# Kernel tuning notes

Measured on AMD Instinct MI355X. Metric: run time of the kernel, lower is better.

Reference implementation:

```python
import jax, jax.numpy as jnp
import numpy as np

B, N_DET, N_T, NY, NX = 4, 128, 2048, 256, 256


def setup_inputs() -> dict:
    key = jax.random.key(0)
    k1, k2, k3 = jax.random.split(key, 3)
    sino = jax.random.normal(k1, (B, 1, N_DET, N_T), dtype=jnp.float32)
    # LUT channel 0: floor temporal index (stored as float, cast to int in forward)
    k_floor = jax.random.randint(k2, (NY, NX, N_DET), 0, N_T).astype(jnp.float32)
    # LUT channel 1: linear interpolation weight alpha in [0,1)
    alpha = jax.random.uniform(k3, (NY, NX, N_DET), dtype=jnp.float32)
    lut = jnp.stack([k_floor, alpha], axis=-1)  # [NY, NX, N_DET, 2]
    return {"sino": sino, "lut": lut}


def reference(sino, lut):
    # sino: [B, 1, n_det, n_t]; lut: [ny, nx, n_det, 2]
    b, c, n_det, n_t = sino.shape
    k_floor = lut[..., 0].astype(jnp.int32)          # [ny, nx, n_det]
    alpha = lut[..., 1]                               # [ny, nx, n_det]
    valid = (k_floor >= 0) & (k_floor < n_t - 1)
    k0 = jnp.clip(k_floor, 0, n_t - 2)
    k1 = k0 + 1
    S = sino[:, 0]                                    # [B, n_det, n_t]
    det = jnp.arange(n_det)                           # broadcasts against [ny,nx,n_det]
    s0 = S[:, det, k0]                                # [B, ny, nx, n_det]
    s1 = S[:, det, k1]                                # [B, ny, nx, n_det]
    sk = (1.0 - alpha) * s0 + alpha * s1
    sk = jnp.where(valid, sk, jnp.zeros_like(sk))
    # Hann apodization window over detectors
    apod = (0.5 - 0.5 * jnp.cos(2.0 * jnp.pi * jnp.arange(n_det, dtype=jnp.float32)
                                / max(n_det - 1, 1))).astype(sino.dtype)
    out = jnp.einsum('bijd,d->bij', sk, apod)
    norm = jnp.maximum(apod.sum(), 1e-06)
    out = out / norm
    return out[:, None]                               # [B, 1, ny, nx]
```

## Files before the change

kernel.cpp:

```cpp
#include <hip/hip_runtime.h>
#include <hip/hip_fp16.h>


#define NB      4
#define NDET    128
#define NT      2048
#define NPIX    65536
#define DPHASE  4
#define DBLOCK  8
#define PTILE   2048
#define THREADS 512
#define PXPT    (PTILE / THREADS)

__global__ __launch_bounds__(THREADS, 4)
void bp_kernel(const float* __restrict__ sino,
               const float* __restrict__ lut,
               float* __restrict__ out) {
    __shared__ __half lds[DPHASE * NT * NB];

    const int tid  = threadIdx.x;
    const int pair = blockIdx.x & 15;
    const int tile = blockIdx.x >> 4;
    const int d0   = pair * DBLOCK;
    const int px0  = tile * PTILE;

    float apod[DBLOCK];
#pragma unroll
    for (int j = 0; j < DBLOCK; ++j) {
        float x = (float)(d0 + j) * (6.28318530717958647692f / 127.0f);
        apod[j] = 0.5f - 0.5f * __cosf(x);
    }

    float acc[PXPT][NB];
#pragma unroll
    for (int i = 0; i < PXPT; ++i)
#pragma unroll
        for (int b = 0; b < NB; ++b) acc[i][b] = 0.0f;

    const float4* sino4 = (const float4*)sino;

    for (int phase = 0; phase < 2; ++phase) {
        const int dg0 = d0 + phase * DPHASE;
        if (phase) __syncthreads();

        for (int f = tid; f < DPHASE * NB * (NT / 4); f += THREADS) {
            int t4 = f & 511;
            int r  = f >> 9;
            int dl = r >> 2;
            int b  = r & 3;
            float4 v = sino4[((size_t)b * NDET + (dg0 + dl)) * (NT / 4) + t4];
            int t = t4 * 4;
            __half* dst = &lds[(dl * NT + t) * NB + b];
            dst[0 * NB] = __float2half(v.x);
            dst[1 * NB] = __float2half(v.y);
            dst[2 * NB] = __float2half(v.z);
            dst[3 * NB] = __float2half(v.w);
        }
        __syncthreads();

#pragma unroll
        for (int i = 0; i < PXPT; ++i) {
            const int px = px0 + tid + i * THREADS;
            const float4* lp = (const float4*)(lut + ((size_t)px * NDET + dg0) * 2);
            float4 L0 = lp[0];
            float4 L1 = lp[1];

            auto do_det = [&](float kf, float af, int dl, int j) {
                int k = (int)kf;
                unsigned uk = (unsigned)k;
                bool valid = uk < 2047u;
                float w  = valid ? apod[j] : 0.0f;
                int  k0  = valid ? k : 0;
                const __half2* q = (const __half2*)&lds[(dl * NT + k0) * NB];
                __half2 s0a = q[0], s0b = q[1];
                __half2 s1a = q[2], s1b = q[3];
                __half2 a2  = __float2half2_rn(af);
                __half2 ska = __hfma2(a2, __hsub2(s1a, s0a), s0a);
                __half2 skb = __hfma2(a2, __hsub2(s1b, s0b), s0b);
                float2 fa = __half22float2(ska);
                float2 fb = __half22float2(skb);
                acc[i][0] = fmaf(w, fa.x, acc[i][0]);
                acc[i][1] = fmaf(w, fa.y, acc[i][1]);
                acc[i][2] = fmaf(w, fb.x, acc[i][2]);
                acc[i][3] = fmaf(w, fb.y, acc[i][3]);
            };
            int jb = phase * DPHASE;
            do_det(L0.x, L0.y, 0, jb + 0);
            do_det(L0.z, L0.w, 1, jb + 1);
            do_det(L1.x, L1.y, 2, jb + 2);
            do_det(L1.z, L1.w, 3, jb + 3);
        }
    }

    const float inv_norm = 1.0f / 63.5f;
#pragma unroll
    for (int i = 0; i < PXPT; ++i) {
        const int px = px0 + tid + i * THREADS;
#pragma unroll
        for (int b = 0; b < NB; ++b) {
            atomicAdd(&out[(size_t)b * NPIX + px], acc[i][b] * inv_norm);
        }
    }
}

extern "C" void kernel_launch(void* const* d_in, const int* in_sizes, int n_in,
                              void* d_out, int out_size, void* d_ws, size_t ws_size,
                              hipStream_t stream) {
    const float* sino = (const float*)d_in[0];
    const float* lut  = (const float*)d_in[1];
    float* out = (float*)d_out;

    hipMemsetAsync(d_out, 0, (size_t)out_size * sizeof(float), stream);

    bp_kernel<<<dim3(512), dim3(THREADS), 0, stream>>>(sino, lut, out);
}
```

Measured before the change: 144.6 us.

## Prefetch LUT across phases, shrink LDS stage, remap blocks to XCDs

Each detector-phase stage now holds 2 detectors instead of 4 (16KB LDS instead of 32KB), which allows more resident blocks per CU. The next phase's LUT float4 is loaded into registers before the current phase's sinogram staging and compute, so the global LUT latency overlaps with LDS fill. Blocks are shrunk to 256 threads and 1024-pixel tiles, the grid is doubled to 1024, and block IDs are remapped so that each XCD handles two detector octets. The costs are four barriers and four sinogram fills per block instead of two, plus extra registers for the prefetched LUT.

```diff
diff --git a/kernel.cpp b/kernel.cpp
--- a/kernel.cpp
+++ b/kernel.cpp
@@ -6,23 +6,27 @@
 #define NDET    128
 #define NT      2048
 #define NPIX    65536
-#define DPHASE  4
-#define DBLOCK  8
-#define PTILE   2048
-#define THREADS 512
+#define DPH     2
+#define NPHASE  4
+#define DBLOCK  (DPH * NPHASE)
+#define PTILE   1024
+#define THREADS 256
 #define PXPT    (PTILE / THREADS)
 
 __global__ __launch_bounds__(THREADS, 4)
 void bp_kernel(const float* __restrict__ sino,
                const float* __restrict__ lut,
                float* __restrict__ out) {
-    __shared__ __half lds[DPHASE * NT * NB];
+    __shared__ __half lds[DPH * NT * NB];
 
-    const int tid  = threadIdx.x;
-    const int pair = blockIdx.x & 15;
-    const int tile = blockIdx.x >> 4;
-    const int d0   = pair * DBLOCK;
-    const int px0  = tile * PTILE;
+    const int tid = threadIdx.x;
+    const int bid   = blockIdx.x;
+    const int xcd   = bid & 7;
+    const int lid   = bid >> 3;
+    const int octet = xcd * 2 + (lid >> 6);
+    const int tile  = lid & 63;
+    const int d0    = octet * DBLOCK;
+    const int px0   = tile * PTILE;
 
     float apod[DBLOCK];
 #pragma unroll
@@ -39,11 +43,26 @@
 
     const float4* sino4 = (const float4*)sino;
 
-    for (int phase = 0; phase < 2; ++phase) {
-        const int dg0 = d0 + phase * DPHASE;
+    auto lut4 = [&](int px, int d) {
+        return (const float4*)(lut + ((size_t)px * NDET + d) * 2);
+    };
+
+    float4 Lcur[PXPT], Lnext[PXPT];
+#pragma unroll
+    for (int i = 0; i < PXPT; ++i)
+        Lcur[i] = *lut4(px0 + tid + i * THREADS, d0);
+
+    for (int phase = 0; phase < NPHASE; ++phase) {
+        const int dg0 = d0 + phase * DPH;
         if (phase) __syncthreads();
 
-        for (int f = tid; f < DPHASE * NB * (NT / 4); f += THREADS) {
+        if (phase + 1 < NPHASE) {
+#pragma unroll
+            for (int i = 0; i < PXPT; ++i)
+                Lnext[i] = *lut4(px0 + tid + i * THREADS, dg0 + DPH);
+        }
+
+        for (int f = tid; f < DPH * NB * (NT / 4); f += THREADS) {
             int t4 = f & 511;
             int r  = f >> 9;
             int dl = r >> 2;
@@ -60,11 +79,7 @@
 
 #pragma unroll
         for (int i = 0; i < PXPT; ++i) {
-            const int px = px0 + tid + i * THREADS;
-            const float4* lp = (const float4*)(lut + ((size_t)px * NDET + dg0) * 2);
-            float4 L0 = lp[0];
-            float4 L1 = lp[1];
-
+            float4 L = Lcur[i];
             auto do_det = [&](float kf, float af, int dl, int j) {
                 int k = (int)kf;
                 unsigned uk = (unsigned)k;
@@ -84,12 +99,11 @@
                 acc[i][2] = fmaf(w, fb.x, acc[i][2]);
                 acc[i][3] = fmaf(w, fb.y, acc[i][3]);
             };
-            int jb = phase * DPHASE;
-            do_det(L0.x, L0.y, 0, jb + 0);
-            do_det(L0.z, L0.w, 1, jb + 1);
-            do_det(L1.x, L1.y, 2, jb + 2);
-            do_det(L1.z, L1.w, 3, jb + 3);
+            do_det(L.x, L.y, 0, phase * DPH + 0);
+            do_det(L.z, L.w, 1, phase * DPH + 1);
         }
+#pragma unroll
+        for (int i = 0; i < PXPT; ++i) Lcur[i] = Lnext[i];
     }
 
     const float inv_norm = 1.0f / 63.5f;
@@ -112,5 +126,5 @@
 
     hipMemsetAsync(d_out, 0, (size_t)out_size * sizeof(float), stream);
 
-    bp_kernel<<<dim3(512), dim3(THREADS), 0, stream>>>(sino, lut, out);
+    bp_kernel<<<dim3(1024), dim3(THREADS), 0, stream>>>(sino, lut, out);
 }
```

Result: slower. 185.6 us (+28.3%).
